# Optimization experiments

Hardware: AMD Instinct MI355X
Metric: run time of the kernel (lower is better)

## Reference

```python
import jax, jax.numpy as jnp
import numpy as np

N = 50000
E = 800000
IN_DIM = 128
HEADS = 4
OUT_DIM = 32
TOT = HEADS * OUT_DIM  # 128 == IN_DIM -> residual_proj is None
LN_EPS = 1e-5
NEG_SLOPE = 0.2


def setup_inputs() -> dict:
    key = jax.random.key(0)
    ks = jax.random.split(key, 10)
    x = jax.random.normal(ks[0], (N, IN_DIM), dtype=jnp.float32)
    # random edges guaranteed src != dst (PyG GATv2Conv removes then re-adds self loops)
    src = jax.random.randint(ks[1], (E,), 0, N)
    off = jax.random.randint(ks[2], (E,), 1, N)
    dst = (src + off) % N
    edge_index = jnp.stack([src, dst]).astype(jnp.int64)
    # glorot-style init for weights
    sc = 1.0 / np.sqrt(IN_DIM)
    W_l = jax.random.uniform(ks[3], (IN_DIM, TOT), jnp.float32, -sc, sc)
    b_l = jnp.zeros((TOT,), jnp.float32)
    W_r = jax.random.uniform(ks[4], (IN_DIM, TOT), jnp.float32, -sc, sc)
    b_r = jnp.zeros((TOT,), jnp.float32)
    att = jax.random.uniform(ks[5], (HEADS, OUT_DIM), jnp.float32, -sc, sc)
    bias = jnp.zeros((TOT,), jnp.float32)
    ln_g = jnp.ones((TOT,), jnp.float32)
    ln_b = jnp.zeros((TOT,), jnp.float32)
    return {"x": x, "edge_index": edge_index, "W_l": W_l, "b_l": b_l,
            "W_r": W_r, "b_r": b_r, "att": att, "bias": bias,
            "ln_g": ln_g, "ln_b": ln_b}


def _gatv2_layer(x, src, dst, W_l, b_l, W_r, b_r, att, bias, ln_g, ln_b):
    n = x.shape[0]
    # GATv2Conv: x_l = lin_l(x) (source/messages), x_r = lin_r(x) (target)
    xl = (x @ W_l + b_l).reshape(n, HEADS, OUT_DIM)
    xr = (x @ W_r + b_r).reshape(n, HEADS, OUT_DIM)
    m = xl[src] + xr[dst]                               # [E+N, H, D]
    s = jnp.einsum('ehd,hd->eh', jax.nn.leaky_relu(m, NEG_SLOPE), att)
    # per-destination softmax (every node has a self loop -> no empty segments)
    smax = jax.ops.segment_max(s, dst, num_segments=n)  # [N, H]
    e = jnp.exp(s - smax[dst])
    denom = jax.ops.segment_sum(e, dst, num_segments=n)
    alpha = e / denom[dst]                              # [E+N, H]
    out = jax.ops.segment_sum(alpha[..., None] * xl[src], dst, num_segments=n)
    out = out.reshape(n, TOT) + bias
    out = out + x                                       # residual (in_dim == total_out_dim)
    mu = jnp.mean(out, axis=-1, keepdims=True)
    var = jnp.mean(jnp.square(out - mu), axis=-1, keepdims=True)
    y = (out - mu) / jnp.sqrt(var + LN_EPS) * ln_g + ln_b
    return jax.nn.elu(y)


def reference(x, edge_index, W_l, b_l, W_r, b_r, att, bias, ln_g, ln_b):
    n = x.shape[0]
    loops = jnp.arange(n, dtype=edge_index.dtype)
    src = jnp.concatenate([edge_index[0], loops])
    dst = jnp.concatenate([edge_index[1], loops])
    return _gatv2_layer(x, src, dst, W_l, b_l, W_r, b_r, att, bias, ln_g, ln_b)
```

## Files before the change

kernel.cpp:

```cpp
#include <hip/hip_runtime.h>

#define N_NODES 50000
#define E_EDGES 800000
#define M_TOTAL (E_EDGES + N_NODES)
#define IN_DIM 128
#define HEADS 4
#define OUT_DIM 32
#define TOT 128
#define LN_EPS 1e-5f
#define NEG_SLOPE 0.2f

#define SCAN_NBLK ((N_NODES + 255) / 256)
#define GEMM_NBLK ((N_NODES + 63) / 64)
#define HIST_NBLK 128
#define EPB 6656
#define HEPB (EPB / 2)
#define SCAT_NBLK (HIST_NBLK * 2)

typedef __bf16 bf16x8 __attribute__((ext_vector_type(8)));
typedef float  f32x4  __attribute__((ext_vector_type(4)));
typedef _Float16 h2   __attribute__((ext_vector_type(2)));

__device__ __forceinline__ float quad_sum(float p) {
    p += __int_as_float(__builtin_amdgcn_update_dpp(
        0, __float_as_int(p), 0xB1 , 0xF, 0xF, true));
    p += __int_as_float(__builtin_amdgcn_update_dpp(
        0, __float_as_int(p), 0x4E , 0xF, 0xF, true));
    return p;
}

__global__ __launch_bounds__(256) void wthist_kernel(
    const int* __restrict__ dsts,
    const float* __restrict__ Wl, const float* __restrict__ Wr,
    unsigned* __restrict__ WT, unsigned char* __restrict__ HP,
    unsigned char* __restrict__ rank8) {
    __shared__ unsigned cnt[N_NODES / 4];
    const int b = blockIdx.x, t = threadIdx.x;
    if (b < 64) {
        const int u = b * 256 + t;
        const int col = u >> 6, k2 = u & 63;
        const float* __restrict__ W = (col < 128) ? Wl : Wr;
        const int c = col & 127;
        union { __bf16 bb[2]; unsigned uu; } p;
        p.bb[0] = (__bf16)W[(2 * k2) * TOT + c];
        p.bb[1] = (__bf16)W[(2 * k2 + 1) * TOT + c];
        WT[col * 64 + k2] = p.uu;
        return;
    }
    const int hb = b - 64;
    const int m_begin = hb * EPB;
    const int m_end = min(m_begin + EPB, M_TOTAL);
    for (int i = t; i < N_NODES / 4; i += 256) cnt[i] = 0;
    __syncthreads();
    for (int m0 = m_begin + t * 4; m0 < m_end; m0 += 1024) {
        int d[4];
        if (m0 < E_EDGES) {
            const int4 dv = *(const int4*)&dsts[m0];
            d[0] = dv.x; d[1] = dv.y; d[2] = dv.z; d[3] = dv.w;
        } else {
            d[0] = m0 - E_EDGES; d[1] = d[0] + 1; d[2] = d[0] + 2; d[3] = d[0] + 3;
        }
        uchar4 r;
        unsigned old, sh;
        sh = (d[0] & 3) * 8; old = atomicAdd(&cnt[d[0] >> 2], 1u << sh);
        r.x = (unsigned char)(old >> sh);
        sh = (d[1] & 3) * 8; old = atomicAdd(&cnt[d[1] >> 2], 1u << sh);
        r.y = (unsigned char)(old >> sh);
        sh = (d[2] & 3) * 8; old = atomicAdd(&cnt[d[2] >> 2], 1u << sh);
        r.z = (unsigned char)(old >> sh);
        sh = (d[3] & 3) * 8; old = atomicAdd(&cnt[d[3] >> 2], 1u << sh);
        r.w = (unsigned char)(old >> sh);
        *(uchar4*)&rank8[m0] = r;
    }
    __syncthreads();
    unsigned* __restrict__ Hrow = (unsigned*)(HP + (size_t)hb * N_NODES);
    for (int i = t; i < N_NODES / 4; i += 256) Hrow[i] = cnt[i];
}

__global__ __launch_bounds__(256) void scan1_kernel(
    unsigned char* __restrict__ HP,
    int* __restrict__ incl, int* __restrict__ blockSums,
    int* __restrict__ degtot) {
    __shared__ int sh[256];
    const int t = threadIdx.x;
    const int i = blockIdx.x * 256 + t;
    int tot = 0;
    if (i < N_NODES) {
        int run = 0;
#pragma unroll 16
        for (int b = 0; b < HIST_NBLK; ++b) {
            const int h = HP[(size_t)b * N_NODES + i];
            HP[(size_t)b * N_NODES + i] = (unsigned char)run;
            run += h;
        }
        tot = run;
        degtot[i] = tot;
    }
    sh[t] = tot;
    __syncthreads();
#pragma unroll
    for (int off = 1; off < 256; off <<= 1) {
        int u = (t >= off) ? sh[t - off] : 0;
        __syncthreads();
        sh[t] += u;
        __syncthreads();
    }
    if (i < N_NODES) incl[i] = sh[t];
    if (t == 255) blockSums[blockIdx.x] = sh[255];
}

__global__ __launch_bounds__(256) void scan23_kernel(
    const int* __restrict__ degtot, const int* __restrict__ blockSums,
    int* __restrict__ rowptr ,
    unsigned short* __restrict__ sorted16) {
    __shared__ int sh[256];
    const int t = threadIdx.x;
    const int v0 = (t < SCAN_NBLK) ? blockSums[t] : 0;
    sh[t] = v0;
    __syncthreads();
#pragma unroll
    for (int off = 1; off < 256; off <<= 1) {
        int u = (t >= off) ? sh[t - off] : 0;
        __syncthreads();
        sh[t] += u;
        __syncthreads();
    }
    const int blockOff = (blockIdx.x == 0) ? 0 : sh[blockIdx.x - 1];
    const int i = blockIdx.x * 256 + t;
    if (i < N_NODES)
        rowptr[i] = blockOff + rowptr[i] - degtot[i];
    if (i == 0) rowptr[N_NODES] = M_TOTAL;
    if (blockIdx.x == 0 && t < 32) sorted16[M_TOTAL + t] = 0;
}

__global__ __launch_bounds__(256) void scattergemm_kernel(
    const int* __restrict__ srcs, const int* __restrict__ dsts,
    const int* __restrict__ rowptr, const unsigned char* __restrict__ P,
    const unsigned char* __restrict__ rank8,
    unsigned short* __restrict__ sorted16,
    const float* __restrict__ x, const unsigned* __restrict__ WT,
    const float* __restrict__ bl, const float* __restrict__ br,
    unsigned* __restrict__ xlb, unsigned* __restrict__ xrb) {
    __shared__ __align__(16) unsigned char smem[N_NODES];
    const int t = threadIdx.x;
    if (blockIdx.x >= GEMM_NBLK) {
        const int sb = blockIdx.x - GEMM_NBLK;
        const int hb = sb >> 1;
        const uint4* __restrict__ Prow = (const uint4*)(P + (size_t)hb * N_NODES);
        for (int i = t; i < N_NODES / 16; i += 256)
            ((uint4*)smem)[i] = Prow[i];
        __syncthreads();
        const int eb = hb * EPB + (sb & 1) * HEPB;
        const int ee = min(eb + HEPB, M_TOTAL);
        for (int m0 = eb + t * 4; m0 < ee; m0 += 1024) {
            int s[4], d[4];
            if (m0 < E_EDGES) {
                const int4 sv = *(const int4*)&srcs[m0];
                const int4 dv = *(const int4*)&dsts[m0];
                s[0] = sv.x; s[1] = sv.y; s[2] = sv.z; s[3] = sv.w;
                d[0] = dv.x; d[1] = dv.y; d[2] = dv.z; d[3] = dv.w;
            } else {
                s[0] = d[0] = m0 - E_EDGES;
                s[1] = d[1] = d[0] + 1; s[2] = d[2] = d[0] + 2; s[3] = d[3] = d[0] + 3;
            }
            const uchar4 r = *(const uchar4*)&rank8[m0];
            sorted16[rowptr[d[0]] + (int)smem[d[0]] + (int)r.x] = (unsigned short)s[0];
            sorted16[rowptr[d[1]] + (int)smem[d[1]] + (int)r.y] = (unsigned short)s[1];
            sorted16[rowptr[d[2]] + (int)smem[d[2]] + (int)r.z] = (unsigned short)s[2];
            sorted16[rowptr[d[3]] + (int)smem[d[3]] + (int)r.w] = (unsigned short)s[3];
        }
        return;
    }
    float (*epi)[16][66] = reinterpret_cast<float(*)[16][66]>(smem);
    const int w = t >> 6, lane = t & 63;
    const int q = lane >> 4, ln = lane & 15;
    const int m0 = blockIdx.x * 64;

    const int row = min(m0 + w * 16 + ln, N_NODES - 1);
    const float* __restrict__ xrow = x + (size_t)row * IN_DIM;
    bf16x8 A[4];
#pragma unroll
    for (int c = 0; c < 4; ++c) {
        const float4 v0 = *(const float4*)&xrow[c * 32 + q * 8];
        const float4 v1 = *(const float4*)&xrow[c * 32 + q * 8 + 4];
        bf16x8 a;
        a[0] = (__bf16)v0.x; a[1] = (__bf16)v0.y; a[2] = (__bf16)v0.z; a[3] = (__bf16)v0.w;
        a[4] = (__bf16)v1.x; a[5] = (__bf16)v1.y; a[6] = (__bf16)v1.z; a[7] = (__bf16)v1.w;
        A[c] = a;
    }

    const int mr = lane >> 2, cg2 = (lane & 3) * 16;
    const int grow = m0 + w * 16 + mr;
#pragma unroll
    for (int g = 0; g < 4; ++g) {
        const int n0 = g * 64;
        const float* __restrict__ bvec = (g < 2) ? bl : br;
        f32x4 acc[4];
#pragma unroll
        for (int nt = 0; nt < 4; ++nt) {
            const float b = bvec[(n0 & 127) + nt * 16 + ln];
            acc[nt] = (f32x4){b, b, b, b};
        }
#pragma unroll
        for (int nt = 0; nt < 4; ++nt) {
            const int col = n0 + nt * 16 + ln;
#pragma unroll
            for (int c = 0; c < 4; ++c) {
                const bf16x8 B = *(const bf16x8*)&WT[col * 64 + c * 16 + q * 4];
                acc[nt] = __builtin_amdgcn_mfma_f32_16x16x32_bf16(A[c], B, acc[nt], 0, 0, 0);
            }
        }
#pragma unroll
        for (int nt = 0; nt < 4; ++nt)
#pragma unroll
            for (int r = 0; r < 4; ++r)
                epi[w][q * 4 + r][nt * 16 + ln] = acc[nt][r];

        if (grow < N_NODES) {
            unsigned p[8];
#pragma unroll
            for (int i = 0; i < 8; ++i) {
                union { _Float16 h[2]; unsigned u; } pk;
                pk.h[0] = (_Float16)epi[w][mr][cg2 + 2 * i];
                pk.h[1] = (_Float16)epi[w][mr][cg2 + 2 * i + 1];
                p[i] = pk.u;
            }
            unsigned* __restrict__ dst = ((g < 2) ? xlb : xrb) +
                (size_t)grow * 64 + (g & 1) * 32 + (cg2 >> 1);
            *(uint4*)&dst[0] = make_uint4(p[0], p[1], p[2], p[3]);
            *(uint4*)&dst[4] = make_uint4(p[4], p[5], p[6], p[7]);
        }
    }
}

__global__ __launch_bounds__(256) void gat_kernel(
    const int* __restrict__ rowptr, const unsigned short* __restrict__ sorted16,
    const unsigned* __restrict__ xlb, const unsigned* __restrict__ xrb,
    const float* __restrict__ att, const float* __restrict__ x,
    const float* __restrict__ bias, const float* __restrict__ g,
    const float* __restrict__ bvec, float* __restrict__ out) {
    const int d = blockIdx.x * 4 + (threadIdx.x >> 6);
    const int lane = threadIdx.x & 63;
    const int ln = lane & 15, q = lane >> 4;
    if (d >= N_NODES) return;

    h2 xrh[4], ath[4];
    {
        const uint4 ur = *(const uint4*)&xrb[(size_t)d * 64 + 4 * ln];
        union { uint4 u; h2 h[4]; } cr; cr.u = ur;
        xrh[0] = cr.h[0]; xrh[1] = cr.h[1]; xrh[2] = cr.h[2]; xrh[3] = cr.h[3];
        const float4 a0 = *(const float4*)&att[8 * ln];
        const float4 a1 = *(const float4*)&att[8 * ln + 4];
        ath[0][0] = (_Float16)a0.x; ath[0][1] = (_Float16)a0.y;
        ath[1][0] = (_Float16)a0.z; ath[1][1] = (_Float16)a0.w;
        ath[2][0] = (_Float16)a1.x; ath[2][1] = (_Float16)a1.y;
        ath[3][0] = (_Float16)a1.z; ath[3][1] = (_Float16)a1.w;
    }
    const h2 slope = (h2){(_Float16)NEG_SLOPE, (_Float16)NEG_SLOPE};
    const int beg = rowptr[d], end = rowptr[d + 1];

    float l = 0.f;
    h2 acc4[4];
#pragma unroll
    for (int k = 0; k < 4; ++k) acc4[k] = (h2){(_Float16)0.f, (_Float16)0.f};

    uint4 u0, u1;
    {
        const int sA0 = (int)sorted16[beg + q];
        const int sA1 = (int)sorted16[beg + 4 + q];
        u0 = *(const uint4*)&xlb[(size_t)sA0 * 64 + 4 * ln];
        u1 = *(const uint4*)&xlb[(size_t)sA1 * 64 + 4 * ln];
    }
    int sB0 = (int)sorted16[beg + 8 + q];
    int sB1 = (int)sorted16[beg + 12 + q];

    for (int base = beg; base < end; base += 8) {
        const int sC0 = (int)sorted16[base + 16 + q];
        const int sC1 = (int)sorted16[base + 20 + q];
        const uint4 un0 = *(const uint4*)&xlb[(size_t)sB0 * 64 + 4 * ln];
        const uint4 un1 = *(const uint4*)&xlb[(size_t)sB1 * 64 + 4 * ln];

        union { unsigned uu; h2 h; } a0, a1, a2, a3, b0, b1, b2, b3;
        a0.uu = u0.x; a1.uu = u0.y; a2.uu = u0.z; a3.uu = u0.w;
        b0.uu = u1.x; b1.uu = u1.y; b2.uu = u1.z; b3.uu = u1.w;
        h2 mA0 = a0.h + xrh[0], mA1 = a1.h + xrh[1];
        h2 mA2 = a2.h + xrh[2], mA3 = a3.h + xrh[3];
        h2 mB0 = b0.h + xrh[0], mB1 = b1.h + xrh[1];
        h2 mB2 = b2.h + xrh[2], mB3 = b3.h + xrh[3];
        mA0 = __builtin_elementwise_max(mA0, mA0 * slope);
        mA1 = __builtin_elementwise_max(mA1, mA1 * slope);
        mA2 = __builtin_elementwise_max(mA2, mA2 * slope);
        mA3 = __builtin_elementwise_max(mA3, mA3 * slope);
        mB0 = __builtin_elementwise_max(mB0, mB0 * slope);
        mB1 = __builtin_elementwise_max(mB1, mB1 * slope);
        mB2 = __builtin_elementwise_max(mB2, mB2 * slope);
        mB3 = __builtin_elementwise_max(mB3, mB3 * slope);
        float p0 = __builtin_amdgcn_fdot2(mA0, ath[0], 0.0f, false);
        p0 = __builtin_amdgcn_fdot2(mA1, ath[1], p0, false);
        p0 = __builtin_amdgcn_fdot2(mA2, ath[2], p0, false);
        p0 = __builtin_amdgcn_fdot2(mA3, ath[3], p0, false);
        float p1 = __builtin_amdgcn_fdot2(mB0, ath[0], 0.0f, false);
        p1 = __builtin_amdgcn_fdot2(mB1, ath[1], p1, false);
        p1 = __builtin_amdgcn_fdot2(mB2, ath[2], p1, false);
        p1 = __builtin_amdgcn_fdot2(mB3, ath[3], p1, false);
        p0 = quad_sum(p0);
        p1 = quad_sum(p1);
        const float e0 = (base + q < end) ? __expf(p0) : 0.f;
        const float e1 = (base + 4 + q < end) ? __expf(p1) : 0.f;
        l += e0 + e1;
        const _Float16 eh0 = (_Float16)e0, eh1 = (_Float16)e1;
        const h2 e20 = (h2){eh0, eh0}, e21 = (h2){eh1, eh1};
        acc4[0] += e20 * a0.h; acc4[0] += e21 * b0.h;
        acc4[1] += e20 * a1.h; acc4[1] += e21 * b1.h;
        acc4[2] += e20 * a2.h; acc4[2] += e21 * b2.h;
        acc4[3] += e20 * a3.h; acc4[3] += e21 * b3.h;

        u0 = un0; u1 = un1; sB0 = sC0; sB1 = sC1;
    }

#pragma unroll
    for (int off = 16; off <= 32; off <<= 1) {
        l += __shfl_xor(l, off, 64);
#pragma unroll
        for (int k = 0; k < 4; ++k) {
            union { h2 h; int i; } tmp; tmp.h = acc4[k];
            tmp.i = __shfl_xor(tmp.i, off, 64);
            acc4[k] += tmp.h;
        }
    }
    float acc[8];
#pragma unroll
    for (int k = 0; k < 4; ++k) {
        acc[2 * k]     = (float)acc4[k][0];
        acc[2 * k + 1] = (float)acc4[k][1];
    }

    const float inv_l = 1.0f / l;
    const float4 xv0 = *(const float4*)&x[(size_t)d * TOT + 8 * ln];
    const float4 xv1 = *(const float4*)&x[(size_t)d * TOT + 8 * ln + 4];
    const float4 bi0 = *(const float4*)&bias[8 * ln];
    const float4 bi1 = *(const float4*)&bias[8 * ln + 4];
    float v[8];
    v[0] = fmaf(acc[0], inv_l, bi0.x + xv0.x);
    v[1] = fmaf(acc[1], inv_l, bi0.y + xv0.y);
    v[2] = fmaf(acc[2], inv_l, bi0.z + xv0.z);
    v[3] = fmaf(acc[3], inv_l, bi0.w + xv0.w);
    v[4] = fmaf(acc[4], inv_l, bi1.x + xv1.x);
    v[5] = fmaf(acc[5], inv_l, bi1.y + xv1.y);
    v[6] = fmaf(acc[6], inv_l, bi1.z + xv1.z);
    v[7] = fmaf(acc[7], inv_l, bi1.w + xv1.w);
    float sum = 0.f, sq = 0.f;
#pragma unroll
    for (int k = 0; k < 8; ++k) { sum += v[k]; sq = fmaf(v[k], v[k], sq); }
#pragma unroll
    for (int off = 1; off <= 8; off <<= 1) {
        sum += __shfl_xor(sum, off, 64);
        sq  += __shfl_xor(sq,  off, 64);
    }
    const float mu  = sum * (1.0f / TOT);
    const float var = sq * (1.0f / TOT) - mu * mu;
    const float inv = rsqrtf(var + LN_EPS);
    const float4 g0 = *(const float4*)&g[8 * ln];
    const float4 g1 = *(const float4*)&g[8 * ln + 4];
    const float4 b0 = *(const float4*)&bvec[8 * ln];
    const float4 b1 = *(const float4*)&bvec[8 * ln + 4];
    float y[8];
    y[0] = (v[0] - mu) * inv * g0.x + b0.x;
    y[1] = (v[1] - mu) * inv * g0.y + b0.y;
    y[2] = (v[2] - mu) * inv * g0.z + b0.z;
    y[3] = (v[3] - mu) * inv * g0.w + b0.w;
    y[4] = (v[4] - mu) * inv * g1.x + b1.x;
    y[5] = (v[5] - mu) * inv * g1.y + b1.y;
    y[6] = (v[6] - mu) * inv * g1.z + b1.z;
    y[7] = (v[7] - mu) * inv * g1.w + b1.w;
#pragma unroll
    for (int k = 0; k < 8; ++k) y[k] = y[k] > 0.f ? y[k] : __expf(y[k]) - 1.f;
    if (q < 2) {
        float4 o = (q == 0) ? make_float4(y[0], y[1], y[2], y[3])
                            : make_float4(y[4], y[5], y[6], y[7]);
        *(float4*)&out[(size_t)d * TOT + 8 * ln + 4 * q] = o;
    }
}

extern "C" void kernel_launch(void* const* d_in, const int* in_sizes, int n_in,
                              void* d_out, int out_size, void* d_ws, size_t ws_size,
                              hipStream_t stream) {
    const float* x    = (const float*)d_in[0];
    const int*   ei   = (const int*)d_in[1];
    const float* Wl   = (const float*)d_in[2];
    const float* bl   = (const float*)d_in[3];
    const float* Wr   = (const float*)d_in[4];
    const float* br   = (const float*)d_in[5];
    const float* att  = (const float*)d_in[6];
    const float* bias = (const float*)d_in[7];
    const float* ln_g = (const float*)d_in[8];
    const float* ln_b = (const float*)d_in[9];
    const int* srcs = ei;
    const int* dsts = ei + E_EDGES;

    unsigned* xlb = (unsigned*)d_ws;
    unsigned* xrb = xlb + (size_t)N_NODES * 64;
    int*   degtot     = (int*)(xrb + (size_t)N_NODES * 64);
    int*   rowptr     = degtot + N_NODES;
    int*   blockSums  = rowptr + N_NODES + 1;
    unsigned* WT      = (unsigned*)(blockSums + SCAN_NBLK + 3);
    unsigned char* HP = (unsigned char*)(WT + 256 * 64);
    unsigned short* sorted16 = (unsigned short*)(HP + (size_t)HIST_NBLK * N_NODES);
    unsigned char*  rank8    = (unsigned char*)(sorted16 + M_TOTAL + 32);

    wthist_kernel<<<64 + HIST_NBLK, 256, 0, stream>>>(dsts, Wl, Wr, WT, HP, rank8);
    scan1_kernel<<<SCAN_NBLK, 256, 0, stream>>>(HP, rowptr, blockSums, degtot);
    scan23_kernel<<<SCAN_NBLK, 256, 0, stream>>>(degtot, blockSums, rowptr, sorted16);
    scattergemm_kernel<<<GEMM_NBLK + SCAT_NBLK, 256, 0, stream>>>(
        srcs, dsts, rowptr, HP, rank8, sorted16, x, WT, bl, br, xlb, xrb);
    gat_kernel<<<(N_NODES + 3) / 4, 256, 0, stream>>>(rowptr, sorted16, xlb, xrb, att, x,
                                                      bias, ln_g, ln_b, (float*)d_out);
}
```

Measured before the change: 184.6 us.

## Co-schedule GEMM with scan1, split scatter into own 512-thread kernel, use exp2

The projection GEMM blocks now launch together with the per-node histogram scan instead of with the edge scatter. The scatter moves into a separate kernel with 512-thread blocks. GEMM blocks no longer reserve the 50KB shared buffer, which may let more of them run per CU. The attention vector is pre-scaled by log2(e) so exp2f can replace __expf in the softmax loop, which adds a small fp16 rounding change to the scores.

```diff
diff --git a/kernel.cpp b/kernel.cpp
--- a/kernel.cpp
+++ b/kernel.cpp
@@ -9,6 +9,7 @@
 #define TOT 128
 #define LN_EPS 1e-5f
 #define NEG_SLOPE 0.2f
+#define LOG2E 1.4426950408889634f
 
 #define SCAN_NBLK ((N_NODES + 255) / 256)
 #define GEMM_NBLK ((N_NODES + 63) / 64)
@@ -77,101 +78,43 @@
     for (int i = t; i < N_NODES / 4; i += 256) Hrow[i] = cnt[i];
 }
 
-__global__ __launch_bounds__(256) void scan1_kernel(
+__global__ __launch_bounds__(256) void scan1gemm_kernel(
     unsigned char* __restrict__ HP,
     int* __restrict__ incl, int* __restrict__ blockSums,
-    int* __restrict__ degtot) {
-    __shared__ int sh[256];
-    const int t = threadIdx.x;
-    const int i = blockIdx.x * 256 + t;
-    int tot = 0;
-    if (i < N_NODES) {
-        int run = 0;
-#pragma unroll 16
-        for (int b = 0; b < HIST_NBLK; ++b) {
-            const int h = HP[(size_t)b * N_NODES + i];
-            HP[(size_t)b * N_NODES + i] = (unsigned char)run;
-            run += h;
-        }
-        tot = run;
-        degtot[i] = tot;
-    }
-    sh[t] = tot;
-    __syncthreads();
-#pragma unroll
-    for (int off = 1; off < 256; off <<= 1) {
-        int u = (t >= off) ? sh[t - off] : 0;
-        __syncthreads();
-        sh[t] += u;
-        __syncthreads();
-    }
-    if (i < N_NODES) incl[i] = sh[t];
-    if (t == 255) blockSums[blockIdx.x] = sh[255];
-}
-
-__global__ __launch_bounds__(256) void scan23_kernel(
-    const int* __restrict__ degtot, const int* __restrict__ blockSums,
-    int* __restrict__ rowptr ,
-    unsigned short* __restrict__ sorted16) {
-    __shared__ int sh[256];
-    const int t = threadIdx.x;
-    const int v0 = (t < SCAN_NBLK) ? blockSums[t] : 0;
-    sh[t] = v0;
-    __syncthreads();
-#pragma unroll
-    for (int off = 1; off < 256; off <<= 1) {
-        int u = (t >= off) ? sh[t - off] : 0;
-        __syncthreads();
-        sh[t] += u;
-        __syncthreads();
-    }
-    const int blockOff = (blockIdx.x == 0) ? 0 : sh[blockIdx.x - 1];
-    const int i = blockIdx.x * 256 + t;
-    if (i < N_NODES)
-        rowptr[i] = blockOff + rowptr[i] - degtot[i];
-    if (i == 0) rowptr[N_NODES] = M_TOTAL;
-    if (blockIdx.x == 0 && t < 32) sorted16[M_TOTAL + t] = 0;
-}
-
-__global__ __launch_bounds__(256) void scattergemm_kernel(
-    const int* __restrict__ srcs, const int* __restrict__ dsts,
-    const int* __restrict__ rowptr, const unsigned char* __restrict__ P,
-    const unsigned char* __restrict__ rank8,
-    unsigned short* __restrict__ sorted16,
+    int* __restrict__ degtot,
     const float* __restrict__ x, const unsigned* __restrict__ WT,
     const float* __restrict__ bl, const float* __restrict__ br,
     unsigned* __restrict__ xlb, unsigned* __restrict__ xrb) {
-    __shared__ __align__(16) unsigned char smem[N_NODES];
+    __shared__ float epi[4][16][66];
     const int t = threadIdx.x;
     if (blockIdx.x >= GEMM_NBLK) {
-        const int sb = blockIdx.x - GEMM_NBLK;
-        const int hb = sb >> 1;
-        const uint4* __restrict__ Prow = (const uint4*)(P + (size_t)hb * N_NODES);
-        for (int i = t; i < N_NODES / 16; i += 256)
-            ((uint4*)smem)[i] = Prow[i];
+        int* sh = (int*)epi;
+        const int i = (blockIdx.x - GEMM_NBLK) * 256 + t;
+        int tot = 0;
+        if (i < N_NODES) {
+            int run = 0;
+#pragma unroll 16
+            for (int b = 0; b < HIST_NBLK; ++b) {
+                const int h = HP[(size_t)b * N_NODES + i];
+                HP[(size_t)b * N_NODES + i] = (unsigned char)run;
+                run += h;
+            }
+            tot = run;
+            degtot[i] = tot;
+        }
+        sh[t] = tot;
         __syncthreads();
-        const int eb = hb * EPB + (sb & 1) * HEPB;
-        const int ee = min(eb + HEPB, M_TOTAL);
-        for (int m0 = eb + t * 4; m0 < ee; m0 += 1024) {
-            int s[4], d[4];
-            if (m0 < E_EDGES) {
-                const int4 sv = *(const int4*)&srcs[m0];
-                const int4 dv = *(const int4*)&dsts[m0];
-                s[0] = sv.x; s[1] = sv.y; s[2] = sv.z; s[3] = sv.w;
-                d[0] = dv.x; d[1] = dv.y; d[2] = dv.z; d[3] = dv.w;
-            } else {
-                s[0] = d[0] = m0 - E_EDGES;
-                s[1] = d[1] = d[0] + 1; s[2] = d[2] = d[0] + 2; s[3] = d[3] = d[0] + 3;
-            }
-            const uchar4 r = *(const uchar4*)&rank8[m0];
-            sorted16[rowptr[d[0]] + (int)smem[d[0]] + (int)r.x] = (unsigned short)s[0];
-            sorted16[rowptr[d[1]] + (int)smem[d[1]] + (int)r.y] = (unsigned short)s[1];
-            sorted16[rowptr[d[2]] + (int)smem[d[2]] + (int)r.z] = (unsigned short)s[2];
-            sorted16[rowptr[d[3]] + (int)smem[d[3]] + (int)r.w] = (unsigned short)s[3];
-        }
+#pragma unroll
+        for (int off = 1; off < 256; off <<= 1) {
+            int u = (t >= off) ? sh[t - off] : 0;
+            __syncthreads();
+            sh[t] += u;
+            __syncthreads();
+        }
+        if (i < N_NODES) incl[i] = sh[t];
+        if (t == 255) blockSums[blockIdx.x - GEMM_NBLK] = sh[255];
         return;
     }
-    float (*epi)[16][66] = reinterpret_cast<float(*)[16][66]>(smem);
     const int w = t >> 6, lane = t & 63;
     const int q = lane >> 4, ln = lane & 15;
     const int m0 = blockIdx.x * 64;
@@ -233,6 +176,64 @@
     }
 }
 
+__global__ __launch_bounds__(256) void scan23_kernel(
+    const int* __restrict__ degtot, const int* __restrict__ blockSums,
+    int* __restrict__ rowptr ,
+    unsigned short* __restrict__ sorted16) {
+    __shared__ int sh[256];
+    const int t = threadIdx.x;
+    const int v0 = (t < SCAN_NBLK) ? blockSums[t] : 0;
+    sh[t] = v0;
+    __syncthreads();
+#pragma unroll
+    for (int off = 1; off < 256; off <<= 1) {
+        int u = (t >= off) ? sh[t - off] : 0;
+        __syncthreads();
+        sh[t] += u;
+        __syncthreads();
+    }
+    const int blockOff = (blockIdx.x == 0) ? 0 : sh[blockIdx.x - 1];
+    const int i = blockIdx.x * 256 + t;
+    if (i < N_NODES)
+        rowptr[i] = blockOff + rowptr[i] - degtot[i];
+    if (i == 0) rowptr[N_NODES] = M_TOTAL;
+    if (blockIdx.x == 0 && t < 32) sorted16[M_TOTAL + t] = 0;
+}
+
+__global__ __launch_bounds__(512) void scatter_kernel(
+    const int* __restrict__ srcs, const int* __restrict__ dsts,
+    const int* __restrict__ rowptr, const unsigned char* __restrict__ P,
+    const unsigned char* __restrict__ rank8,
+    unsigned short* __restrict__ sorted16) {
+    __shared__ __align__(16) unsigned char smem[N_NODES];
+    const int t = threadIdx.x;
+    const int sb = blockIdx.x;
+    const int hb = sb >> 1;
+    const uint4* __restrict__ Prow = (const uint4*)(P + (size_t)hb * N_NODES);
+    for (int i = t; i < N_NODES / 16; i += 512)
+        ((uint4*)smem)[i] = Prow[i];
+    __syncthreads();
+    const int eb = hb * EPB + (sb & 1) * HEPB;
+    const int ee = min(eb + HEPB, M_TOTAL);
+    for (int m0 = eb + t * 4; m0 < ee; m0 += 2048) {
+        int s[4], d[4];
+        if (m0 < E_EDGES) {
+            const int4 sv = *(const int4*)&srcs[m0];
+            const int4 dv = *(const int4*)&dsts[m0];
+            s[0] = sv.x; s[1] = sv.y; s[2] = sv.z; s[3] = sv.w;
+            d[0] = dv.x; d[1] = dv.y; d[2] = dv.z; d[3] = dv.w;
+        } else {
+            s[0] = d[0] = m0 - E_EDGES;
+            s[1] = d[1] = d[0] + 1; s[2] = d[2] = d[0] + 2; s[3] = d[3] = d[0] + 3;
+        }
+        const uchar4 r = *(const uchar4*)&rank8[m0];
+        sorted16[rowptr[d[0]] + (int)smem[d[0]] + (int)r.x] = (unsigned short)s[0];
+        sorted16[rowptr[d[1]] + (int)smem[d[1]] + (int)r.y] = (unsigned short)s[1];
+        sorted16[rowptr[d[2]] + (int)smem[d[2]] + (int)r.z] = (unsigned short)s[2];
+        sorted16[rowptr[d[3]] + (int)smem[d[3]] + (int)r.w] = (unsigned short)s[3];
+    }
+}
+
 __global__ __launch_bounds__(256) void gat_kernel(
     const int* __restrict__ rowptr, const unsigned short* __restrict__ sorted16,
     const unsigned* __restrict__ xlb, const unsigned* __restrict__ xrb,
@@ -251,10 +252,10 @@
         xrh[0] = cr.h[0]; xrh[1] = cr.h[1]; xrh[2] = cr.h[2]; xrh[3] = cr.h[3];
         const float4 a0 = *(const float4*)&att[8 * ln];
         const float4 a1 = *(const float4*)&att[8 * ln + 4];
-        ath[0][0] = (_Float16)a0.x; ath[0][1] = (_Float16)a0.y;
-        ath[1][0] = (_Float16)a0.z; ath[1][1] = (_Float16)a0.w;
-        ath[2][0] = (_Float16)a1.x; ath[2][1] = (_Float16)a1.y;
-        ath[3][0] = (_Float16)a1.z; ath[3][1] = (_Float16)a1.w;
+        ath[0][0] = (_Float16)(a0.x * LOG2E); ath[0][1] = (_Float16)(a0.y * LOG2E);
+        ath[1][0] = (_Float16)(a0.z * LOG2E); ath[1][1] = (_Float16)(a0.w * LOG2E);
+        ath[2][0] = (_Float16)(a1.x * LOG2E); ath[2][1] = (_Float16)(a1.y * LOG2E);
+        ath[3][0] = (_Float16)(a1.z * LOG2E); ath[3][1] = (_Float16)(a1.w * LOG2E);
     }
     const h2 slope = (h2){(_Float16)NEG_SLOPE, (_Float16)NEG_SLOPE};
     const int beg = rowptr[d], end = rowptr[d + 1];
@@ -305,8 +306,8 @@
         p1 = __builtin_amdgcn_fdot2(mB3, ath[3], p1, false);
         p0 = quad_sum(p0);
         p1 = quad_sum(p1);
-        const float e0 = (base + q < end) ? __expf(p0) : 0.f;
-        const float e1 = (base + 4 + q < end) ? __expf(p1) : 0.f;
+        const float e0 = (base + q < end) ? exp2f(p0) : 0.f;
+        const float e1 = (base + 4 + q < end) ? exp2f(p1) : 0.f;
         l += e0 + e1;
         const _Float16 eh0 = (_Float16)e0, eh1 = (_Float16)e1;
         const h2 e20 = (h2){eh0, eh0}, e21 = (h2){eh1, eh1};
@@ -409,10 +410,10 @@
     unsigned char*  rank8    = (unsigned char*)(sorted16 + M_TOTAL + 32);
 
     wthist_kernel<<<64 + HIST_NBLK, 256, 0, stream>>>(dsts, Wl, Wr, WT, HP, rank8);
-    scan1_kernel<<<SCAN_NBLK, 256, 0, stream>>>(HP, rowptr, blockSums, degtot);
+    scan1gemm_kernel<<<GEMM_NBLK + SCAN_NBLK, 256, 0, stream>>>(
+        HP, rowptr, blockSums, degtot, x, WT, bl, br, xlb, xrb);
     scan23_kernel<<<SCAN_NBLK, 256, 0, stream>>>(degtot, blockSums, rowptr, sorted16);
-    scattergemm_kernel<<<GEMM_NBLK + SCAT_NBLK, 256, 0, stream>>>(
-        srcs, dsts, rowptr, HP, rank8, sorted16, x, WT, bl, br, xlb, xrb);
+    scatter_kernel<<<SCAT_NBLK, 512, 0, stream>>>(srcs, dsts, rowptr, HP, rank8, sorted16);
     gat_kernel<<<(N_NODES + 3) / 4, 256, 0, stream>>>(rowptr, sorted16, xlb, xrb, att, x,
                                                       bias, ln_g, ln_b, (float*)d_out);
 }
```

Result: slower. 188.6 us (+2.2%).
